# Optimization experiments

Measured on AMD Instinct MI355X. Metric: run time of the kernel, lower is better.

The kernel has to match this reference:

```python
import jax, jax.numpy as jnp
import numpy as np

N = 20000; E = 320000; IN = 512; H = 4; C = 128; HC = H * C; SD = 2; SE = 128
NEG = 0.01      # nn.LeakyReLU default slope (post-norm activations)
ATT_NEG = 0.2   # GATv2 attention LeakyReLU slope


def _gatv2(x, wl, bl, wr, br, att, bias, src, dst, concat):
    # PyG GATv2Conv (eval mode, add_self_loops already applied to src/dst)
    n = x.shape[0]
    xl = (x @ wl.T + bl).reshape(n, H, C)   # source-side projection
    xr = (x @ wr.T + br).reshape(n, H, C)   # target-side projection
    e = jax.nn.leaky_relu(xl[src] + xr[dst], ATT_NEG)        # [Etot, H, C]
    logits = jnp.einsum('ehc,hc->eh', e, att)                # [Etot, H]
    m = jax.ops.segment_max(logits, dst, num_segments=n)     # segment softmax over dst
    ez = jnp.exp(logits - m[dst])
    denom = jax.ops.segment_sum(ez, dst, num_segments=n)
    alpha = ez / denom[dst]
    out = jax.ops.segment_sum(xl[src] * alpha[:, :, None], dst, num_segments=n)  # [n, H, C]
    out = out.reshape(n, HC) if concat else out.mean(axis=1)
    return out + bias, alpha


def _bn(x, g, b):
    # BatchNorm1d, training-mode batch statistics (biased variance), eps=1e-5
    mu = x.mean(0)
    v = x.var(0)
    return g * (x - mu) * jax.lax.rsqrt(v + 1e-5) + b


def setup_inputs() -> dict:
    key = jax.random.key(0)
    ks = jax.random.split(key, 20)
    p = lambda i, shape: jax.random.normal(ks[i], shape, jnp.float32) * 0.05
    return dict(
        x=jax.random.normal(ks[0], (N, IN), jnp.float32),
        edge_index=jax.random.randint(ks[1], (2, E), 0, N),
        spatial_coords=jax.random.uniform(ks[2], (N, SD), dtype=jnp.float32),
        w1_l=p(3, (HC, IN)), b1_l=jnp.zeros((HC,)), w1_r=p(4, (HC, IN)), b1_r=jnp.zeros((HC,)),
        att1=p(5, (H, C)), bias1=jnp.zeros((HC,)), bn1_g=jnp.ones((HC,)), bn1_b=jnp.zeros((HC,)),
        w2_l=p(6, (HC, HC)), b2_l=jnp.zeros((HC,)), w2_r=p(7, (HC, HC)), b2_r=jnp.zeros((HC,)),
        att2=p(8, (H, C)), bias2=jnp.zeros((HC,)), bn2_g=jnp.ones((HC,)), bn2_b=jnp.zeros((HC,)),
        w3_l=p(9, (HC, HC)), b3_l=jnp.zeros((HC,)), w3_r=p(10, (HC, HC)), b3_r=jnp.zeros((HC,)),
        att3=p(11, (H, C)), bias3=jnp.zeros((C,)), bn3_g=jnp.ones((C,)), bn3_b=jnp.zeros((C,)),
        sp_w1=p(12, (SE, SD)), sp_b1=jnp.zeros((SE,)),
        sp_w2=p(13, (C, SE)), sp_b2=jnp.zeros((C,)),
        mha_in_w=p(14, (3 * SE, SE)), mha_in_b=jnp.zeros((3 * SE,)),
        mha_out_w=p(15, (SE, SE)), mha_out_b=jnp.zeros((SE,)),
        gate_w=p(16, (1, 2 * C)), gate_b=jnp.zeros((1,)),
    )


def reference(x, edge_index, spatial_coords,
              w1_l, b1_l, w1_r, b1_r, att1, bias1, bn1_g, bn1_b,
              w2_l, b2_l, w2_r, b2_r, att2, bias2, bn2_g, bn2_b,
              w3_l, b3_l, w3_r, b3_r, att3, bias3, bn3_g, bn3_b,
              sp_w1, sp_b1, sp_w2, sp_b2,
              mha_in_w, mha_in_b, mha_out_w, mha_out_b,
              gate_w, gate_b):
    loop = jnp.arange(N)
    src = jnp.concatenate([edge_index[0], loop])  # add self loops (PyG default)
    dst = jnp.concatenate([edge_index[1], loop])

    h1, a1 = _gatv2(x, w1_l, b1_l, w1_r, b1_r, att1, bias1, src, dst, True)
    h1 = jax.nn.leaky_relu(_bn(h1, bn1_g, bn1_b), NEG)
    h2, a2 = _gatv2(h1, w2_l, b2_l, w2_r, b2_r, att2, bias2, src, dst, True)
    h2 = jax.nn.leaky_relu(_bn(h2, bn2_g, bn2_b), NEG)
    z, a3 = _gatv2(h2, w3_l, b3_l, w3_r, b3_r, att3, bias3, src, dst, False)
    z = jax.nn.leaky_relu(_bn(z, bn3_g, bn3_b), NEG)

    # spatial embedding MLP (Linear -> LeakyReLU -> Linear -> LeakyReLU)
    emb = jax.nn.leaky_relu(spatial_coords @ sp_w1.T + sp_b1, NEG)
    emb = jax.nn.leaky_relu(emb @ sp_w2.T + sp_b2, NEG)
    # MultiheadAttention over a length-1 sequence: softmax over a single key is 1,
    # so output = W_o (W_v e + b_v) + b_o
    wv = mha_in_w[2 * SE:]
    bv = mha_in_b[2 * SE:]
    sp = (emb @ wv.T + bv) @ mha_out_w.T + mha_out_b  # [N, C]

    gate = jax.nn.softmax(jnp.concatenate([z, sp], axis=-1) @ gate_w.T + gate_b, axis=-1)  # [N,1] (all ones: size-1 softmax, faithful to source)
    z = gate * z + (1.0 - gate) * sp
    return z, a1, a2, a3, gate
```

## Files before the change

kernel.cpp:

```cpp
#include <hip/hip_runtime.h>
#include <math.h>

#define NN 20000
#define EE 320000
#define ETOT 340000
#define DEGCAP 128

typedef __attribute__((ext_vector_type(8))) short short8;
typedef __attribute__((ext_vector_type(4))) float f32x4;

__device__ __forceinline__ float lrelu(float x, float s) { return fmaxf(x, s * x); }
__device__ __forceinline__ float bf2f(ushort u) {
    union { uint i; float f; } c;
    c.i = ((uint)u) << 16;
    return c.f;
}
__device__ __forceinline__ ushort f2bf(float f) {
    uint u = __float_as_uint(f);
    uint r = (u + 0x7FFFu + ((u >> 16) & 1u)) >> 16;
    return (ushort)r;
}
__device__ __forceinline__ void gload16(const ushort* g, ushort* l) {
    __builtin_amdgcn_global_load_lds((const __attribute__((address_space(1))) void*)g,
                                     (__attribute__((address_space(3))) void*)l, 16, 0, 0);
}

__global__ void k_count(const int* __restrict__ ei, int* __restrict__ counts) {
    int i = blockIdx.x * blockDim.x + threadIdx.x;
    if (i >= ETOT) return;
    int d = (i < EE) ? ei[EE + i] : (i - EE);
    atomicAdd(&counts[d], 1);
}

__global__ __launch_bounds__(1024) void k_scan(const int* __restrict__ counts, int* __restrict__ rstart) {
    __shared__ int sm[1024];
    int t = threadIdx.x;
    const int CH = 20;
    int base = t * CH;
    int loc[CH];
    int s = 0;
#pragma unroll
    for (int j = 0; j < CH; ++j) {
        int idx = base + j;
        int v = (idx < NN) ? counts[idx] : 0;
        loc[j] = s;
        s += v;
    }
    sm[t] = s;
    __syncthreads();
    for (int o = 1; o < 1024; o <<= 1) {
        int v = (t >= o) ? sm[t - o] : 0;
        __syncthreads();
        if (t >= o) sm[t] += v;
        __syncthreads();
    }
    int off = sm[t] - s;
#pragma unroll
    for (int j = 0; j < CH; ++j) {
        int idx = base + j;
        if (idx < NN) rstart[idx] = off + loc[j];
    }
    if (t == 1023) rstart[NN] = sm[1023];
}

__global__ void k_scatter(const int* __restrict__ ei, const int* __restrict__ rstart,
                          int* __restrict__ cursor, int* __restrict__ csr) {
    int i = blockIdx.x * blockDim.x + threadIdx.x;
    if (i >= ETOT) return;
    int d = (i < EE) ? ei[EE + i] : (i - EE);
    int pos = atomicAdd(&cursor[d], 1);
    csr[rstart[d] + pos] = i;
}

__global__ void k_cast(const float* __restrict__ in, ushort* __restrict__ out, int n) {
    int i = (blockIdx.x * blockDim.x + threadIdx.x) * 4;
    if (i >= n) return;
    float4 v = *(const float4*)(in + i);
    uint2 pk;
    pk.x = (uint)f2bf(v.x) | ((uint)f2bf(v.y) << 16);
    pk.y = (uint)f2bf(v.z) | ((uint)f2bf(v.w) << 16);
    *(uint2*)(out + i) = pk;
}

__global__ void k_castw(const float* __restrict__ w0, const float* __restrict__ w1, const float* __restrict__ w2,
                        const float* __restrict__ w3, const float* __restrict__ w4, const float* __restrict__ w5,
                        ushort* __restrict__ out) {
    int i = blockIdx.x * blockDim.x + threadIdx.x;
    if (i >= 6 * 65536) return;
    int which = i >> 16;
    int off = (i & 65535) << 2;
    const float* src = which == 0 ? w0 : which == 1 ? w1 : which == 2 ? w2 : which == 3 ? w3 : which == 4 ? w4 : w5;
    float4 v = *(const float4*)(src + off);
    uint2 pk;
    pk.x = (uint)f2bf(v.x) | ((uint)f2bf(v.y) << 16);
    pk.y = (uint)f2bf(v.z) | ((uint)f2bf(v.w) << 16);
    *(uint2*)(out + which * 262144 + off) = pk;
}

__global__ __launch_bounds__(256) void k_gemm2(const ushort* __restrict__ A, const ushort* __restrict__ W,
                                               const float* __restrict__ bl, const float* __restrict__ br,
                                               ushort* __restrict__ XL, ushort* __restrict__ XR) {
    __shared__ ushort As[4][128][8];
    __shared__ ushort Bs[4][128][8];
    int tid = threadIdx.x;
    int wid = tid >> 6, lane = tid & 63;
    int wm = wid >> 1, wn = wid & 1;
    int bid = blockIdx.x;
    int L = (bid & 7) * 157 + (bid >> 3);
    int mt = L >> 3, nt = L & 7;
    int bm = mt * 128, bn = nt * 128;
    const float* bias = (nt >= 4) ? br : bl;
    ushort* C = (nt >= 4) ? XR : XL;
    int cb = bn - ((nt >= 4) ? 512 : 0);
    int lrow = lane & 15, lslot = lane >> 4;
    int f0 = tid, f1 = tid + 256;
    int r0 = f0 & 127, ks0 = f0 >> 7;
    int r1 = f1 & 127, ks1 = f1 >> 7;
    int ar0 = bm + r0; if (ar0 >= NN) ar0 = NN - 1;
    int ar1 = bm + r1; if (ar1 >= NN) ar1 = NN - 1;
    const ushort* ga0 = A + (size_t)ar0 * 512 + ks0 * 8;
    const ushort* ga1 = A + (size_t)ar1 * 512 + ks1 * 8;
    const ushort* gb0 = W + (size_t)(bn + r0) * 512 + ks0 * 8;
    const ushort* gb1 = W + (size_t)(bn + r1) * 512 + ks1 * 8;
    ushort* lA = &As[0][0][0];
    ushort* lB = &Bs[0][0][0];
    ushort* lA0 = lA + (size_t)(wid * 64) * 8;
    ushort* lA1 = lA + (size_t)(256 + wid * 64) * 8;
    ushort* lB0 = lB + (size_t)(wid * 64) * 8;
    ushort* lB1 = lB + (size_t)(256 + wid * 64) * 8;
    f32x4 acc[4][4] = {};
    for (int k0 = 0; k0 < 512; k0 += 32) {
        gload16(ga0 + k0, lA0);
        gload16(ga1 + k0, lA1);
        gload16(gb0 + k0, lB0);
        gload16(gb1 + k0, lB1);
        __syncthreads();
        short8 af[4], bfr[4];
#pragma unroll
        for (int i = 0; i < 4; ++i) af[i] = *(const short8*)&As[lslot][wm * 64 + i * 16 + lrow][0];
#pragma unroll
        for (int j = 0; j < 4; ++j) bfr[j] = *(const short8*)&Bs[lslot][wn * 64 + j * 16 + lrow][0];
#pragma unroll
        for (int i = 0; i < 4; ++i)
#pragma unroll
            for (int j = 0; j < 4; ++j)
                acc[i][j] = __builtin_amdgcn_mfma_f32_16x16x32_bf16(af[i], bfr[j], acc[i][j], 0, 0, 0);
        __syncthreads();
    }
#pragma unroll
    for (int i = 0; i < 4; ++i) {
#pragma unroll
        for (int j = 0; j < 4; ++j) {
            int gcol = cb + wn * 64 + j * 16 + lrow;
            float bv = bias[gcol];
            int growb = bm + wm * 64 + i * 16 + lslot * 4;
#pragma unroll
            for (int reg = 0; reg < 4; ++reg) {
                int grow = growb + reg;
                if (grow < NN) C[(size_t)grow * 512 + gcol] = f2bf(acc[i][j][reg] + bv);
            }
        }
    }
}

__global__ __launch_bounds__(256) void k_fused(const ushort* __restrict__ xl, const ushort* __restrict__ xr,
                                               const float* __restrict__ att, const int* __restrict__ ei,
                                               const int* __restrict__ rstart, const int* __restrict__ csr,
                                               const float* __restrict__ bias, float* __restrict__ alpha,
                                               ushort* __restrict__ dest, int meanHeads) {
    __shared__ float slg[4][DEGCAP][4];
    __shared__ int ssrc[4][DEGCAP];
    int w = threadIdx.x >> 6, lane = threadIdx.x & 63;
    int node = blockIdx.x * 4 + w;
    int s0 = rstart[node];
    int deg = rstart[node + 1] - s0;
    int hh = lane >> 4;
    short8 xrv = *(const short8*)(xr + (size_t)node * 512 + lane * 8);
    const float4* at = (const float4*)att + lane * 2;
    float4 a0 = at[0], a1 = at[1];
    float attv[8] = {a0.x, a0.y, a0.z, a0.w, a1.x, a1.y, a1.z, a1.w};
    float xrf[8];
#pragma unroll
    for (int j = 0; j < 8; ++j) xrf[j] = bf2f((ushort)xrv[j]);
    for (int i = lane; i < deg; i += 64) {
        int e = csr[s0 + i];
        ssrc[w][i < DEGCAP ? i : 0] = (e < EE) ? ei[e] : e - EE;
    }
    float m = -1e30f, denom = 0.f;
    float acc[8] = {};
    int scur = ssrc[w][0];
    short8 row = *(const short8*)(xl + (size_t)scur * 512 + lane * 8);
    for (int i = 0; i < deg; ++i) {
        short8 rown = row;
        if (i + 1 < deg) {
            int sn = ssrc[w][(i + 1) < DEGCAP ? (i + 1) : 0];
            rown = *(const short8*)(xl + (size_t)sn * 512 + lane * 8);
        }
        float rf[8];
#pragma unroll
        for (int j = 0; j < 8; ++j) rf[j] = bf2f((ushort)row[j]);
        float p = 0.f;
#pragma unroll
        for (int j = 0; j < 8; ++j) {
            float e = rf[j] + xrf[j];
            p = fmaf(fmaxf(e, 0.2f * e), attv[j], p);
        }
        p += __shfl_xor(p, 1);
        p += __shfl_xor(p, 2);
        p += __shfl_xor(p, 4);
        p += __shfl_xor(p, 8);
        if ((lane & 15) == 0 && i < DEGCAP) slg[w][i][hh] = p;
        if (p <= m) {
            float wg = __expf(p - m);
            denom += wg;
#pragma unroll
            for (int j = 0; j < 8; ++j) acc[j] = fmaf(wg, rf[j], acc[j]);
        } else {
            float sc = __expf(m - p);
            denom = fmaf(denom, sc, 1.f);
#pragma unroll
            for (int j = 0; j < 8; ++j) acc[j] = fmaf(acc[j], sc, rf[j]);
            m = p;
        }
        row = rown;
    }
    float rd = 1.f / denom;
    float m0 = __shfl(m, 0), m1 = __shfl(m, 16), m2 = __shfl(m, 32), m3 = __shfl(m, 48);
    float r0 = __shfl(rd, 0), r1 = __shfl(rd, 16), r2 = __shfl(rd, 32), r3 = __shfl(rd, 48);
    int nal = deg < DEGCAP ? deg : DEGCAP;
    for (int i = lane; i < nal; i += 64) {
        int e = csr[s0 + i];
        float4 l = *(const float4*)&slg[w][i][0];
        float4 av;
        av.x = __expf(l.x - m0) * r0;
        av.y = __expf(l.y - m1) * r1;
        av.z = __expf(l.z - m2) * r2;
        av.w = __expf(l.w - m3) * r3;
        *(float4*)(alpha + (size_t)e * 4) = av;
    }
#pragma unroll
    for (int j = 0; j < 8; ++j) acc[j] *= rd;
    if (!meanHeads) {
        int c = lane * 8;
        short8 o;
#pragma unroll
        for (int j = 0; j < 8; ++j) o[j] = (short)f2bf(acc[j] + bias[c + j]);
        *(short8*)(dest + (size_t)node * 512 + c) = o;
    } else {
#pragma unroll
        for (int j = 0; j < 8; ++j) {
            acc[j] += __shfl_xor(acc[j], 16);
            acc[j] += __shfl_xor(acc[j], 32);
        }
        if (lane < 16) {
            int c = lane * 8;
            short8 o;
#pragma unroll
            for (int j = 0; j < 8; ++j) o[j] = (short)f2bf(0.25f * acc[j] + bias[c + j]);
            *(short8*)(dest + (size_t)node * 128 + c) = o;
        }
    }
}

__global__ void k_bnstats(const ushort* __restrict__ X, float* __restrict__ s, float* __restrict__ s2, int npairs) {
    int t = threadIdx.x;
    if (t >= npairs) return;
    float a0 = 0.f, a1 = 0.f, q0 = 0.f, q1 = 0.f;
    for (int r = blockIdx.x; r < NN; r += gridDim.x) {
        uint p = ((const uint*)X)[r * npairs + t];
        float v0 = bf2f((ushort)(p & 0xffffu));
        float v1 = bf2f((ushort)(p >> 16));
        a0 += v0; q0 += v0 * v0;
        a1 += v1; q1 += v1 * v1;
    }
    atomicAdd(&s[2 * t], a0);
    atomicAdd(&s[2 * t + 1], a1);
    atomicAdd(&s2[2 * t], q0);
    atomicAdd(&s2[2 * t + 1], q1);
}

__global__ void k_bnfin(const float* __restrict__ s, const float* __restrict__ s2, float* __restrict__ mu,
                        float* __restrict__ rs, int ncols) {
    int c = threadIdx.x;
    if (c < ncols) {
        float m = s[c] * (1.f / NN);
        float v = s2[c] * (1.f / NN) - m * m;
        mu[c] = m;
        rs[c] = rsqrtf(v + 1e-5f);
    }
}

__global__ void k_bnapply(const ushort* __restrict__ X, const float* __restrict__ g, const float* __restrict__ b,
                          const float* __restrict__ mu, const float* __restrict__ rs, float* __restrict__ Yf,
                          ushort* __restrict__ Yb, int mask4, int n4) {
    int i = blockIdx.x * blockDim.x + threadIdx.x;
    if (i >= n4) return;
    int c = (i & mask4) << 2;
    uint2 p = ((const uint2*)X)[i];
    float x0 = bf2f((ushort)(p.x & 0xffffu)), x1 = bf2f((ushort)(p.x >> 16));
    float x2 = bf2f((ushort)(p.y & 0xffffu)), x3 = bf2f((ushort)(p.y >> 16));
    float4 G = *(const float4*)(g + c);
    float4 B = *(const float4*)(b + c);
    float4 M = *(const float4*)(mu + c);
    float4 R = *(const float4*)(rs + c);
    float4 y;
    y.x = lrelu(G.x * (x0 - M.x) * R.x + B.x, 0.01f);
    y.y = lrelu(G.y * (x1 - M.y) * R.y + B.y, 0.01f);
    y.z = lrelu(G.z * (x2 - M.z) * R.z + B.z, 0.01f);
    y.w = lrelu(G.w * (x3 - M.w) * R.w + B.w, 0.01f);
    if (Yb) {
        uint2 pk;
        pk.x = (uint)f2bf(y.x) | ((uint)f2bf(y.y) << 16);
        pk.y = (uint)f2bf(y.z) | ((uint)f2bf(y.w) << 16);
        *(uint2*)(Yb + (size_t)i * 4) = pk;
    } else {
        ((float4*)Yf)[i] = y;
    }
}

__global__ void k_gate(float* __restrict__ g) {
    int i = blockIdx.x * blockDim.x + threadIdx.x;
    if (i < NN) g[i] = 1.0f;
}

extern "C" void kernel_launch(void* const* d_in, const int* in_sizes, int n_in,
                              void* d_out, int out_size, void* d_ws, size_t ws_size,
                              hipStream_t stream) {
    const float* x = (const float*)d_in[0];
    const int* ei = (const int*)d_in[1];
    const float* wl[3] = {(const float*)d_in[3], (const float*)d_in[11], (const float*)d_in[19]};
    const float* bl[3] = {(const float*)d_in[4], (const float*)d_in[12], (const float*)d_in[20]};
    const float* wr[3] = {(const float*)d_in[5], (const float*)d_in[13], (const float*)d_in[21]};
    const float* br[3] = {(const float*)d_in[6], (const float*)d_in[14], (const float*)d_in[22]};
    const float* att[3] = {(const float*)d_in[7], (const float*)d_in[15], (const float*)d_in[23]};
    const float* bias[3] = {(const float*)d_in[8], (const float*)d_in[16], (const float*)d_in[24]};
    const float* bng[3] = {(const float*)d_in[9], (const float*)d_in[17], (const float*)d_in[25]};
    const float* bnb[3] = {(const float*)d_in[10], (const float*)d_in[18], (const float*)d_in[26]};

    ushort* a_bf = (ushort*)d_ws;
    ushort* xl_bf = a_bf + (size_t)NN * 512;
    ushort* xr_bf = xl_bf + (size_t)NN * 512;
    ushort* h_bf = xr_bf + (size_t)NN * 512;
    ushort* wbuf = h_bf + (size_t)NN * 512;
    float* fp = (float*)(wbuf + 6 * 262144);
    float* bsum = fp;
    float* bsq = bsum + 512;
    float* bmu = bsq + 512;
    float* brs = bmu + 512;
    int* counts = (int*)(brs + 512);
    int* cursor = counts + NN;
    int* rstart = cursor + NN;
    int* csr = rstart + (NN + 1);
    size_t need = (size_t)((char*)(csr + ETOT) - (char*)d_ws);
    if (ws_size < need) return;

    float* out = (float*)d_out;
    float* zout = out;
    float* aout[3] = {out + 2560000, out + 3920000, out + 5280000};
    float* gout = out + 6640000;

    hipMemsetAsync(counts, 0, 2 * NN * sizeof(int), stream);
    k_count<<<(ETOT + 255) / 256, 256, 0, stream>>>(ei, counts);
    k_scan<<<1, 1024, 0, stream>>>(counts, rstart);
    k_scatter<<<(ETOT + 255) / 256, 256, 0, stream>>>(ei, rstart, cursor, csr);

    k_cast<<<(NN * 512 / 4 + 255) / 256, 256, 0, stream>>>(x, a_bf, NN * 512);
    k_castw<<<(6 * 65536 + 255) / 256, 256, 0, stream>>>(wl[0], wr[0], wl[1], wr[1], wl[2], wr[2], wbuf);

    for (int l = 0; l < 3; ++l) {
        const ushort* wb = wbuf + (size_t)l * 524288;
        k_gemm2<<<1256, 256, 0, stream>>>(a_bf, wb, bl[l], br[l], xl_bf, xr_bf);
        int ncols = (l == 2) ? 128 : 512;
        k_fused<<<NN / 4, 256, 0, stream>>>(xl_bf, xr_bf, att[l], ei, rstart, csr, bias[l], aout[l], h_bf,
                                            (l == 2) ? 1 : 0);
        hipMemsetAsync(bsum, 0, 1024 * sizeof(float), stream);
        k_bnstats<<<240, 256, 0, stream>>>(h_bf, bsum, bsq, ncols / 2);
        k_bnfin<<<1, ncols, 0, stream>>>(bsum, bsq, bmu, brs, ncols);
        int n4 = NN * ncols / 4;
        if (l < 2) {
            k_bnapply<<<(n4 + 255) / 256, 256, 0, stream>>>(h_bf, bng[l], bnb[l], bmu, brs, nullptr, a_bf,
                                                            ncols / 4 - 1, n4);
        } else {
            k_bnapply<<<(n4 + 255) / 256, 256, 0, stream>>>(h_bf, bng[l], bnb[l], bmu, brs, zout, nullptr,
                                                            ncols / 4 - 1, n4);
        }
    }
    k_gate<<<(NN + 255) / 256, 256, 0, stream>>>(gout);
}
```

Measured before the change: 677.3 us.

## Double-buffer GEMM LDS loads and merge small prep/BN/gate kernels

```diff
diff --git a/kernel.cpp b/kernel.cpp
--- a/kernel.cpp
+++ b/kernel.cpp
@@ -23,13 +23,6 @@
 __device__ __forceinline__ void gload16(const ushort* g, ushort* l) {
     __builtin_amdgcn_global_load_lds((const __attribute__((address_space(1))) void*)g,
                                      (__attribute__((address_space(3))) void*)l, 16, 0, 0);
-}
-
-__global__ void k_count(const int* __restrict__ ei, int* __restrict__ counts) {
-    int i = blockIdx.x * blockDim.x + threadIdx.x;
-    if (i >= ETOT) return;
-    int d = (i < EE) ? ei[EE + i] : (i - EE);
-    atomicAdd(&counts[d], 1);
 }
 
 __global__ __launch_bounds__(1024) void k_scan(const int* __restrict__ counts, int* __restrict__ rstart) {
@@ -72,36 +65,42 @@
     csr[rstart[d] + pos] = i;
 }
 
-__global__ void k_cast(const float* __restrict__ in, ushort* __restrict__ out, int n) {
-    int i = (blockIdx.x * blockDim.x + threadIdx.x) * 4;
-    if (i >= n) return;
-    float4 v = *(const float4*)(in + i);
-    uint2 pk;
-    pk.x = (uint)f2bf(v.x) | ((uint)f2bf(v.y) << 16);
-    pk.y = (uint)f2bf(v.z) | ((uint)f2bf(v.w) << 16);
-    *(uint2*)(out + i) = pk;
-}
-
-__global__ void k_castw(const float* __restrict__ w0, const float* __restrict__ w1, const float* __restrict__ w2,
-                        const float* __restrict__ w3, const float* __restrict__ w4, const float* __restrict__ w5,
-                        ushort* __restrict__ out) {
-    int i = blockIdx.x * blockDim.x + threadIdx.x;
-    if (i >= 6 * 65536) return;
-    int which = i >> 16;
-    int off = (i & 65535) << 2;
-    const float* src = which == 0 ? w0 : which == 1 ? w1 : which == 2 ? w2 : which == 3 ? w3 : which == 4 ? w4 : w5;
-    float4 v = *(const float4*)(src + off);
-    uint2 pk;
-    pk.x = (uint)f2bf(v.x) | ((uint)f2bf(v.y) << 16);
-    pk.y = (uint)f2bf(v.z) | ((uint)f2bf(v.w) << 16);
-    *(uint2*)(out + which * 262144 + off) = pk;
+__global__ void k_prep(const float* __restrict__ x, const float* __restrict__ w0, const float* __restrict__ w1,
+                       const float* __restrict__ w2, const float* __restrict__ w3, const float* __restrict__ w4,
+                       const float* __restrict__ w5, ushort* __restrict__ xout, ushort* __restrict__ wout,
+                       const int* __restrict__ ei, int* __restrict__ counts) {
+    int b = blockIdx.x, t = threadIdx.x;
+    if (b < 10000) {
+        int i = (b * 256 + t) * 4;
+        float4 v = *(const float4*)(x + i);
+        uint2 pk;
+        pk.x = (uint)f2bf(v.x) | ((uint)f2bf(v.y) << 16);
+        pk.y = (uint)f2bf(v.z) | ((uint)f2bf(v.w) << 16);
+        *(uint2*)(xout + i) = pk;
+    } else if (b < 11536) {
+        int q = (b - 10000) * 256 + t;
+        if (q >= 6 * 65536) return;
+        int which = q >> 16;
+        int off = (q & 65535) << 2;
+        const float* src = which == 0 ? w0 : which == 1 ? w1 : which == 2 ? w2 : which == 3 ? w3 : which == 4 ? w4 : w5;
+        float4 v = *(const float4*)(src + off);
+        uint2 pk;
+        pk.x = (uint)f2bf(v.x) | ((uint)f2bf(v.y) << 16);
+        pk.y = (uint)f2bf(v.z) | ((uint)f2bf(v.w) << 16);
+        *(uint2*)(wout + which * 262144 + off) = pk;
+    } else {
+        int i = (b - 11536) * 256 + t;
+        if (i >= ETOT) return;
+        int d = (i < EE) ? ei[EE + i] : (i - EE);
+        atomicAdd(&counts[d], 1);
+    }
 }
 
 __global__ __launch_bounds__(256) void k_gemm2(const ushort* __restrict__ A, const ushort* __restrict__ W,
                                                const float* __restrict__ bl, const float* __restrict__ br,
                                                ushort* __restrict__ XL, ushort* __restrict__ XR) {
-    __shared__ ushort As[4][128][8];
-    __shared__ ushort Bs[4][128][8];
+    __shared__ ushort As[2][512][8];
+    __shared__ ushort Bs[2][512][8];
     int tid = threadIdx.x;
     int wid = tid >> 6, lane = tid & 63;
     int wm = wid >> 1, wn = wid & 1;
@@ -122,30 +121,33 @@
     const ushort* ga1 = A + (size_t)ar1 * 512 + ks1 * 8;
     const ushort* gb0 = W + (size_t)(bn + r0) * 512 + ks0 * 8;
     const ushort* gb1 = W + (size_t)(bn + r1) * 512 + ks1 * 8;
-    ushort* lA = &As[0][0][0];
-    ushort* lB = &Bs[0][0][0];
-    ushort* lA0 = lA + (size_t)(wid * 64) * 8;
-    ushort* lA1 = lA + (size_t)(256 + wid * 64) * 8;
-    ushort* lB0 = lB + (size_t)(wid * 64) * 8;
-    ushort* lB1 = lB + (size_t)(256 + wid * 64) * 8;
     f32x4 acc[4][4] = {};
-    for (int k0 = 0; k0 < 512; k0 += 32) {
-        gload16(ga0 + k0, lA0);
-        gload16(ga1 + k0, lA1);
-        gload16(gb0 + k0, lB0);
-        gload16(gb1 + k0, lB1);
+    gload16(ga0, &As[0][f0][0]);
+    gload16(ga1, &As[0][f1][0]);
+    gload16(gb0, &Bs[0][f0][0]);
+    gload16(gb1, &Bs[0][f1][0]);
+#pragma unroll 4
+    for (int t = 0; t < 16; ++t) {
+        int cur = t & 1;
         __syncthreads();
+        if (t < 15) {
+            int k0 = (t + 1) * 32;
+            int nxt = cur ^ 1;
+            gload16(ga0 + k0, &As[nxt][f0][0]);
+            gload16(ga1 + k0, &As[nxt][f1][0]);
+            gload16(gb0 + k0, &Bs[nxt][f0][0]);
+            gload16(gb1 + k0, &Bs[nxt][f1][0]);
+        }
         short8 af[4], bfr[4];
 #pragma unroll
-        for (int i = 0; i < 4; ++i) af[i] = *(const short8*)&As[lslot][wm * 64 + i * 16 + lrow][0];
-#pragma unroll
-        for (int j = 0; j < 4; ++j) bfr[j] = *(const short8*)&Bs[lslot][wn * 64 + j * 16 + lrow][0];
+        for (int i = 0; i < 4; ++i) af[i] = *(const short8*)&As[cur][lslot * 128 + wm * 64 + i * 16 + lrow][0];
+#pragma unroll
+        for (int j = 0; j < 4; ++j) bfr[j] = *(const short8*)&Bs[cur][lslot * 128 + wn * 64 + j * 16 + lrow][0];
 #pragma unroll
         for (int i = 0; i < 4; ++i)
 #pragma unroll
             for (int j = 0; j < 4; ++j)
                 acc[i][j] = __builtin_amdgcn_mfma_f32_16x16x32_bf16(af[i], bfr[j], acc[i][j], 0, 0, 0);
-        __syncthreads();
     }
 #pragma unroll
     for (int i = 0; i < 4; ++i) {
@@ -279,35 +281,31 @@
     atomicAdd(&s2[2 * t + 1], q1);
 }
 
-__global__ void k_bnfin(const float* __restrict__ s, const float* __restrict__ s2, float* __restrict__ mu,
-                        float* __restrict__ rs, int ncols) {
-    int c = threadIdx.x;
-    if (c < ncols) {
-        float m = s[c] * (1.f / NN);
-        float v = s2[c] * (1.f / NN) - m * m;
-        mu[c] = m;
-        rs[c] = rsqrtf(v + 1e-5f);
-    }
-}
-
 __global__ void k_bnapply(const ushort* __restrict__ X, const float* __restrict__ g, const float* __restrict__ b,
-                          const float* __restrict__ mu, const float* __restrict__ rs, float* __restrict__ Yf,
-                          ushort* __restrict__ Yb, int mask4, int n4) {
+                          const float* __restrict__ bsum, const float* __restrict__ bsq, float* __restrict__ Yf,
+                          ushort* __restrict__ Yb, float* __restrict__ gout, int mask4, int n4) {
     int i = blockIdx.x * blockDim.x + threadIdx.x;
+    if (gout && i < NN) gout[i] = 1.0f;
     if (i >= n4) return;
     int c = (i & mask4) << 2;
     uint2 p = ((const uint2*)X)[i];
     float x0 = bf2f((ushort)(p.x & 0xffffu)), x1 = bf2f((ushort)(p.x >> 16));
     float x2 = bf2f((ushort)(p.y & 0xffffu)), x3 = bf2f((ushort)(p.y >> 16));
+    float4 S = *(const float4*)(bsum + c);
+    float4 Q = *(const float4*)(bsq + c);
     float4 G = *(const float4*)(g + c);
     float4 B = *(const float4*)(b + c);
-    float4 M = *(const float4*)(mu + c);
-    float4 R = *(const float4*)(rs + c);
+    const float inv = 1.f / NN;
+    float mx = S.x * inv, my = S.y * inv, mz = S.z * inv, mw = S.w * inv;
+    float rx = rsqrtf(Q.x * inv - mx * mx + 1e-5f);
+    float ry = rsqrtf(Q.y * inv - my * my + 1e-5f);
+    float rz = rsqrtf(Q.z * inv - mz * mz + 1e-5f);
+    float rw = rsqrtf(Q.w * inv - mw * mw + 1e-5f);
     float4 y;
-    y.x = lrelu(G.x * (x0 - M.x) * R.x + B.x, 0.01f);
-    y.y = lrelu(G.y * (x1 - M.y) * R.y + B.y, 0.01f);
-    y.z = lrelu(G.z * (x2 - M.z) * R.z + B.z, 0.01f);
-    y.w = lrelu(G.w * (x3 - M.w) * R.w + B.w, 0.01f);
+    y.x = lrelu(G.x * (x0 - mx) * rx + B.x, 0.01f);
+    y.y = lrelu(G.y * (x1 - my) * ry + B.y, 0.01f);
+    y.z = lrelu(G.z * (x2 - mz) * rz + B.z, 0.01f);
+    y.w = lrelu(G.w * (x3 - mw) * rw + B.w, 0.01f);
     if (Yb) {
         uint2 pk;
         pk.x = (uint)f2bf(y.x) | ((uint)f2bf(y.y) << 16);
@@ -316,11 +314,6 @@
     } else {
         ((float4*)Yf)[i] = y;
     }
-}
-
-__global__ void k_gate(float* __restrict__ g) {
-    int i = blockIdx.x * blockDim.x + threadIdx.x;
-    if (i < NN) g[i] = 1.0f;
 }
 
 extern "C" void kernel_launch(void* const* d_in, const int* in_sizes, int n_in,
@@ -345,9 +338,7 @@
     float* fp = (float*)(wbuf + 6 * 262144);
     float* bsum = fp;
     float* bsq = bsum + 512;
-    float* bmu = bsq + 512;
-    float* brs = bmu + 512;
-    int* counts = (int*)(brs + 512);
+    int* counts = (int*)(bsq + 512);
     int* cursor = counts + NN;
     int* rstart = cursor + NN;
     int* csr = rstart + (NN + 1);
@@ -360,12 +351,9 @@
     float* gout = out + 6640000;
 
     hipMemsetAsync(counts, 0, 2 * NN * sizeof(int), stream);
-    k_count<<<(ETOT + 255) / 256, 256, 0, stream>>>(ei, counts);
+    k_prep<<<12865, 256, 0, stream>>>(x, wl[0], wr[0], wl[1], wr[1], wl[2], wr[2], a_bf, wbuf, ei, counts);
     k_scan<<<1, 1024, 0, stream>>>(counts, rstart);
     k_scatter<<<(ETOT + 255) / 256, 256, 0, stream>>>(ei, rstart, cursor, csr);
-
-    k_cast<<<(NN * 512 / 4 + 255) / 256, 256, 0, stream>>>(x, a_bf, NN * 512);
-    k_castw<<<(6 * 65536 + 255) / 256, 256, 0, stream>>>(wl[0], wr[0], wl[1], wr[1], wl[2], wr[2], wbuf);
 
     for (int l = 0; l < 3; ++l) {
         const ushort* wb = wbuf + (size_t)l * 524288;
@@ -375,15 +363,13 @@
                                             (l == 2) ? 1 : 0);
         hipMemsetAsync(bsum, 0, 1024 * sizeof(float), stream);
         k_bnstats<<<240, 256, 0, stream>>>(h_bf, bsum, bsq, ncols / 2);
-        k_bnfin<<<1, ncols, 0, stream>>>(bsum, bsq, bmu, brs, ncols);
         int n4 = NN * ncols / 4;
         if (l < 2) {
-            k_bnapply<<<(n4 + 255) / 256, 256, 0, stream>>>(h_bf, bng[l], bnb[l], bmu, brs, nullptr, a_bf,
-                                                            ncols / 4 - 1, n4);
+            k_bnapply<<<(n4 + 255) / 256, 256, 0, stream>>>(h_bf, bng[l], bnb[l], bsum, bsq, nullptr, a_bf,
+                                                            nullptr, ncols / 4 - 1, n4);
         } else {
-            k_bnapply<<<(n4 + 255) / 256, 256, 0, stream>>>(h_bf, bng[l], bnb[l], bmu, brs, zout, nullptr,
-                                                            ncols / 4 - 1, n4);
-        }
-    }
-    k_gate<<<(NN + 255) / 256, 256, 0, stream>>>(gout);
-}
+            k_bnapply<<<(n4 + 255) / 256, 256, 0, stream>>>(h_bf, bng[l], bnb[l], bsum, bsq, zout, nullptr,
+                                                            gout, ncols / 4 - 1, n4);
+        }
+    }
+}
```

Result: slower. 702.9 us (+3.8%).
